# Kernel tuning notes

Hardware: AMD Instinct MI355X
Metric: run time of the kernel (lower is better)

## Reference

```python
import jax, jax.numpy as jnp
import numpy as np
import math

D_MODEL = 1024
NUM_HEADS = 16
D_FF = 4096
EPS = 1e-5
BATCH = 2
SEQ = 2048


def _trunc_normal(key, shape, std):
    # truncated normal on [-3std, 3std], matching nn.init.trunc_normal_
    return std * jax.random.truncated_normal(key, -3.0, 3.0, shape, dtype=jnp.float32)


def setup_inputs() -> dict:
    key = jax.random.key(0)
    ks = jax.random.split(key, 8)
    x = jax.random.normal(ks[0], (BATCH, SEQ, D_MODEL), dtype=jnp.float32)
    std_dd = math.sqrt(2.0 / (D_MODEL + D_MODEL))
    std_up = math.sqrt(2.0 / (D_MODEL + D_FF))
    # Linear stores W as [out_features, in_features]; forward does x @ W.T
    W_q = _trunc_normal(ks[1], (D_MODEL, D_MODEL), std_dd)
    W_k = _trunc_normal(ks[2], (D_MODEL, D_MODEL), std_dd)
    W_v = _trunc_normal(ks[3], (D_MODEL, D_MODEL), std_dd)
    W_o = _trunc_normal(ks[4], (D_MODEL, D_MODEL), std_dd)
    W1 = _trunc_normal(ks[5], (D_FF, D_MODEL), std_up)
    W2 = _trunc_normal(ks[6], (D_MODEL, D_FF), std_up)
    ln1_w = jnp.ones((D_MODEL,), jnp.float32)
    ln1_b = jnp.zeros((D_MODEL,), jnp.float32)
    ln2_w = jnp.ones((D_MODEL,), jnp.float32)
    ln2_b = jnp.zeros((D_MODEL,), jnp.float32)
    return {"x": x, "W_q": W_q, "W_k": W_k, "W_v": W_v, "W_o": W_o,
            "W1": W1, "W2": W2,
            "ln1_w": ln1_w, "ln1_b": ln1_b, "ln2_w": ln2_w, "ln2_b": ln2_b}


def _layernorm(x, w, b):
    xf = x.astype(jnp.float32)
    mean = xf.mean(axis=-1, keepdims=True)
    var = jnp.mean((xf - mean) ** 2, axis=-1, keepdims=True)
    xn = (xf - mean) / jnp.sqrt(var + EPS)
    return (xn * w.astype(jnp.float32) + b.astype(jnp.float32)).astype(x.dtype)


def _attention(x, W_q, W_k, W_v, W_o):
    B, S, D = x.shape
    H, dk = NUM_HEADS, D // NUM_HEADS
    Q = (x @ W_q.T).reshape(B, S, H, dk).transpose(0, 2, 1, 3)  # [B,H,S,dk]
    K = (x @ W_k.T).reshape(B, S, H, dk).transpose(0, 2, 1, 3)
    V = (x @ W_v.T).reshape(B, S, H, dk).transpose(0, 2, 1, 3)
    scores = jnp.einsum('bhqd,bhkd->bhqk', Q, K) / math.sqrt(dk)
    causal = jnp.tril(jnp.ones((S, S), dtype=bool))
    scores = jnp.where(causal, scores, -jnp.inf)
    attn = jax.nn.softmax(scores, axis=-1)
    out = jnp.einsum('bhqk,bhkd->bhqd', attn, V)  # [B,H,S,dk]
    out = out.transpose(0, 2, 1, 3).reshape(B, S, D)
    return out @ W_o.T


def _ffn(x, W1, W2):
    h = x @ W1.T
    h = h * (h > 0)  # ReLU
    return h @ W2.T


def reference(x, W_q, W_k, W_v, W_o, W1, W2, ln1_w, ln1_b, ln2_w, ln2_b):
    x = x + _attention(_layernorm(x, ln1_w, ln1_b), W_q, W_k, W_v, W_o)
    x = x + _ffn(_layernorm(x, ln2_w, ln2_b), W1, W2)
    return x
```

## Files before the change

kernel.cpp:

```cpp
#include <hip/hip_runtime.h>
#include <stdint.h>

typedef unsigned short u16;
typedef unsigned int u32;
typedef __bf16 bf16x8 __attribute__((ext_vector_type(8)));
typedef float f32x4 __attribute__((ext_vector_type(4)));
typedef unsigned short u16x8 __attribute__((ext_vector_type(8)));
typedef unsigned short u16x4 __attribute__((ext_vector_type(4)));
typedef u16x8 u16x8_a __attribute__((may_alias));
typedef u16x4 u16x4_a __attribute__((may_alias));

#define DEV static __device__ __forceinline__

DEV u16 f2bf(float f) {
  unsigned u = __builtin_bit_cast(unsigned, f);
  u += 0x7fffu + ((u >> 16) & 1u);
  return (u16)(u >> 16);
}
DEV bf16x8 ld8(const u16* p) {
  u16x8 v = *(const u16x8_a*)p;
  return __builtin_bit_cast(bf16x8, v);
}
DEV f32x4 vmax4(f32x4 a, f32x4 b) {
  f32x4 r;
  r[0] = fmaxf(a[0], b[0]); r[1] = fmaxf(a[1], b[1]);
  r[2] = fmaxf(a[2], b[2]); r[3] = fmaxf(a[3], b[3]);
  return r;
}
DEV void swz_block(int& bx, int& by) {
  const int gx = gridDim.x;
  const int nwg = gx * gridDim.y;
  int lin = by * gx + bx;
  const int q = nwg >> 3, r = nwg & 7, x = lin & 7, p = lin >> 3;
  lin = (x < r ? x * (q + 1) : r * (q + 1) + (x - r) * q) + p;
  bx = lin % gx; by = lin / gx;
}

#define GL_LDS16(gp, lp)                                                        \
  __builtin_amdgcn_global_load_lds(                                             \
      (const __attribute__((address_space(1))) void*)(gp),                      \
      (__attribute__((address_space(3))) void*)(lp), 16, 0, 0)

#define VMW4 asm volatile("s_waitcnt vmcnt(4)" ::: "memory")
#define VMW2 asm volatile("s_waitcnt vmcnt(2)" ::: "memory")
#define VMW0 asm volatile("s_waitcnt vmcnt(0)" ::: "memory")
#define BAR  __builtin_amdgcn_s_barrier()

struct Cvt6 {
  const float* s[6];
  u16* d[6];
  int n4[6];
};
__global__ __launch_bounds__(256) void cvt6_k(Cvt6 c) {
  const int yi = blockIdx.y;
  const int i = blockIdx.x * 256 + threadIdx.x;
  if (i < c.n4[yi]) {
    float4 v = ((const float4*)c.s[yi])[i];
    u16x4 o;
    o[0] = f2bf(v.x); o[1] = f2bf(v.y); o[2] = f2bf(v.z); o[3] = f2bf(v.w);
    *(u16x4_a*)(c.d[yi] + (size_t)i * 4) = o;
  }
}

__global__ __launch_bounds__(256) void ln_k(const float* __restrict__ x,
                                            const float* __restrict__ w,
                                            const float* __restrict__ b,
                                            u16* __restrict__ o) {
  const int row = blockIdx.x, t = threadIdx.x;
  const float4 v = ((const float4*)(x + (size_t)row * 1024))[t];
  float s = v.x + v.y + v.z + v.w;
  float q = v.x * v.x + v.y * v.y + v.z * v.z + v.w * v.w;
#pragma unroll
  for (int m = 1; m < 64; m <<= 1) { s += __shfl_xor(s, m); q += __shfl_xor(q, m); }
  __shared__ float ss[4], qq[4];
  if ((t & 63) == 0) { ss[t >> 6] = s; qq[t >> 6] = q; }
  __syncthreads();
  s = ss[0] + ss[1] + ss[2] + ss[3];
  q = qq[0] + qq[1] + qq[2] + qq[3];
  const float mean = s * (1.f / 1024.f);
  const float var = q * (1.f / 1024.f) - mean * mean;
  const float rstd = rsqrtf(var + 1e-5f);
  const float4 wv = ((const float4*)w)[t];
  const float4 bv = ((const float4*)b)[t];
  u16x4 ov;
  ov[0] = f2bf((v.x - mean) * rstd * wv.x + bv.x);
  ov[1] = f2bf((v.y - mean) * rstd * wv.y + bv.y);
  ov[2] = f2bf((v.z - mean) * rstd * wv.z + bv.z);
  ov[3] = f2bf((v.w - mean) * rstd * wv.w + bv.w);
  *(u16x4_a*)(o + (size_t)row * 1024 + t * 4) = ov;
}

__global__ __launch_bounds__(256) void vtr_k(const u16* __restrict__ qkvV,
                                             u16* __restrict__ vt) {
  __shared__ u16 T[64][65];
  const int st = blockIdx.x, bh = blockIdx.y;
  const int b = bh >> 4, h = bh & 15;
  const int t = threadIdx.x;
  const u16* src = qkvV + ((size_t)(b * 2048 + st * 64)) * 3072 + h * 64;
  const int r = t >> 2, c0 = (t & 3) * 16;
  u16x8 a0 = *(const u16x8_a*)(src + (size_t)r * 3072 + c0);
  u16x8 a1 = *(const u16x8_a*)(src + (size_t)r * 3072 + c0 + 8);
#pragma unroll
  for (int e = 0; e < 8; ++e) { T[r][c0 + e] = a0[e]; T[r][c0 + 8 + e] = a1[e]; }
  __syncthreads();
  const int d = t >> 2, s0 = (t & 3) * 16;
  u16x8 o0, o1;
#pragma unroll
  for (int e = 0; e < 8; ++e) { o0[e] = T[s0 + e][d]; o1[e] = T[s0 + 8 + e][d]; }
  u16* dst = vt + ((size_t)bh * 64 + d) * 2048 + (size_t)st * 64 + s0;
  *(u16x8_a*)dst = o0;
  *(u16x8_a*)(dst + 8) = o1;
}

DEV void stage_op(const u16* __restrict__ G, int K, int kk, u16* lds, int set,
                  int isB, int w, int l) {
#pragma unroll
  for (int i = 0; i < 2; ++i) {
    const int c = i * 8 + w;
    int rb;
    if (!isB) { const int lr = c * 8; rb = (lr < 64 ? lr : lr + 64) + set * 64; }
    else      { rb = (c >> 2) * 64 + set * 32 + (c & 3) * 8; }
    const int row = rb + (l >> 3);
    const int c8 = (l & 7) ^ (row & 7);
    GL_LDS16(G + (size_t)row * K + kk + c8 * 8, lds + rb * 64);
  }
}
DEV void rdA(const u16* as, int wr, int mh, int l15, int l4, bf16x8 af[4][2]) {
#pragma unroll
  for (int f = 0; f < 4; ++f) {
    const int row = wr * 128 + mh * 64 + f * 16 + l15;
#pragma unroll
    for (int ks = 0; ks < 2; ++ks) {
      const int c8 = (ks * 4 + l4) ^ (row & 7);
      af[f][ks] = ld8(as + row * 64 + c8 * 8);
    }
  }
}
DEV void rdB(const u16* bs, int wc, int nh, int l15, int l4, bf16x8 bf_[2][2]) {
#pragma unroll
  for (int g = 0; g < 2; ++g) {
    const int row = wc * 64 + nh * 32 + g * 16 + l15;
#pragma unroll
    for (int ks = 0; ks < 2; ++ks) {
      const int c8 = (ks * 4 + l4) ^ (row & 7);
      bf_[g][ks] = ld8(bs + row * 64 + c8 * 8);
    }
  }
}

#define MFMA16(mh, nh)                                                          \
  __builtin_amdgcn_s_setprio(1);                                                \
  _Pragma("unroll")                                                             \
  for (int f = 0; f < 4; ++f) {                                                 \
    _Pragma("unroll")                                                           \
    for (int g = 0; g < 2; ++g) {                                               \
      f32x4& a_ = acc[(mh) * 4 + f][(nh) * 2 + g];                              \
      a_ = __builtin_amdgcn_mfma_f32_16x16x32_bf16(af[f][0], bfr[g][0], a_, 0, 0, 0); \
      a_ = __builtin_amdgcn_mfma_f32_16x16x32_bf16(af[f][1], bfr[g][1], a_, 0, 0, 0); \
    }                                                                           \
  }                                                                             \
  __builtin_amdgcn_s_setprio(0);

template <int EPI>
__global__ __launch_bounds__(512, 2) void gemm8(const u16* __restrict__ A,
                                                const u16* __restrict__ Bw,
                                                u16* __restrict__ Cp,
                                                int M, int N, int K, int qcols) {
  __shared__ __align__(16) u16 As[2][256 * 64];
  __shared__ __align__(16) u16 Bs[2][256 * 64];
  const int t = threadIdx.x, w = t >> 6, l = t & 63;
  const int l15 = l & 15, l4 = l >> 4;
  const int wr = w >> 2, wc = w & 3;
  int bx = blockIdx.x, by = blockIdx.y;
  swz_block(bx, by);
  const int bm0 = by * 256, bn0 = bx * 256;
  const u16* Ab = A + (size_t)bm0 * K;
  const u16* Bb = Bw + (size_t)bn0 * K;

  f32x4 acc[8][4] = {};
  stage_op(Ab, K, 0, As[0], 0, 0, w, l);
  stage_op(Bb, K, 0, Bs[0], 0, 1, w, l);
  stage_op(Bb, K, 0, Bs[0], 1, 1, w, l);
  stage_op(Ab, K, 0, As[0], 1, 0, w, l);
  VMW4;
  BAR;

  const int nk = K >> 6;
  int cur = 0;
  bf16x8 af[4][2], bfr[2][2];
  for (int kt = 0; kt < nk; ++kt) {
    const int kn = (kt + 1) << 6;
    const bool more = (kt + 1 < nk);
    u16* An = As[cur ^ 1];
    u16* Bn = Bs[cur ^ 1];
    rdA(As[cur], wr, 0, l15, l4, af);
    rdB(Bs[cur], wc, 0, l15, l4, bfr);
    if (more) stage_op(Ab, K, kn, An, 0, 0, w, l);
    BAR;
    MFMA16(0, 0)
    if (more) { VMW4; } else { VMW2; }
    BAR;
    rdB(Bs[cur], wc, 1, l15, l4, bfr);
    if (more) stage_op(Bb, K, kn, Bn, 0, 1, w, l);
    BAR;
    MFMA16(0, 1)
    if (more) { VMW4; } else { VMW0; }
    BAR;
    rdA(As[cur], wr, 1, l15, l4, af);
    if (more) stage_op(Bb, K, kn, Bn, 1, 1, w, l);
    BAR;
    MFMA16(1, 1)
    BAR;
    rdB(Bs[cur], wc, 0, l15, l4, bfr);
    if (more) stage_op(Ab, K, kn, An, 1, 0, w, l);
    BAR;
    MFMA16(1, 0)
    if (more) { VMW4; }
    BAR;
    cur ^= 1;
  }

#pragma unroll
  for (int m = 0; m < 8; ++m) {
    const int row0 = bm0 + wr * 128 + m * 16 + l4 * 4;
#pragma unroll
    for (int n = 0; n < 4; ++n) {
      const int col = bn0 + wc * 64 + n * 16 + l15;
      const float qs = (col < qcols) ? 0.18033688f : 1.f;
#pragma unroll
      for (int r = 0; r < 4; ++r) {
        float v = acc[m][n][r] * qs;
        if constexpr (EPI == 1) v = v > 0.f ? v : 0.f;
        Cp[(size_t)(row0 + r) * N + col] = f2bf(v);
      }
    }
  }
}

__global__ __launch_bounds__(256, 2) void gemm64(const u16* __restrict__ A,
                                                 const u16* __restrict__ Bw,
                                                 float* __restrict__ C,
                                                 const float* __restrict__ res,
                                                 int M, int N, int K) {
  __shared__ __align__(16) u16 As[2][64 * 64];
  __shared__ __align__(16) u16 Bs[2][128 * 64];
  const int t = threadIdx.x, w = t >> 6, l = t & 63;
  const int l15 = l & 15, l4 = l >> 4;
  const int wr = w >> 1, wc = w & 1;
  int bx = blockIdx.x, by = blockIdx.y;
  swz_block(bx, by);
  const int bm0 = by * 64, bn0 = bx * 128;
  const u16* Ab = A + (size_t)bm0 * K;
  const u16* Bb = Bw + (size_t)bn0 * K;

  auto stgA = [&](int buf, int kk) {
#pragma unroll
    for (int i = 0; i < 2; ++i) {
      const int s = t + i * 256;
      const int row = s >> 3;
      const int c8 = (l & 7) ^ (row & 7);
      GL_LDS16(Ab + (size_t)row * K + kk + c8 * 8, &As[buf][(s >> 6) * 512]);
    }
  };
  auto stgB = [&](int buf, int kk) {
#pragma unroll
    for (int i = 0; i < 4; ++i) {
      const int s = t + i * 256;
      const int row = s >> 3;
      const int c8 = (l & 7) ^ (row & 7);
      GL_LDS16(Bb + (size_t)row * K + kk + c8 * 8, &Bs[buf][(s >> 6) * 512]);
    }
  };

  f32x4 acc[2][4] = {};
  stgA(0, 0); stgB(0, 0);
  const int nk = K >> 6;
  int cur = 0;
  for (int kt = 0; kt < nk; ++kt) {
    __syncthreads();
    if (kt + 1 < nk) { stgA(cur ^ 1, (kt + 1) << 6); stgB(cur ^ 1, (kt + 1) << 6); }
    bf16x8 af[2][2], bfr[4][2];
#pragma unroll
    for (int f = 0; f < 2; ++f) {
      const int row = wr * 32 + f * 16 + l15;
#pragma unroll
      for (int ks = 0; ks < 2; ++ks)
        af[f][ks] = ld8(&As[cur][row * 64 + (((ks * 4 + l4) ^ (row & 7)) * 8)]);
    }
#pragma unroll
    for (int n = 0; n < 4; ++n) {
      const int row = wc * 64 + n * 16 + l15;
#pragma unroll
      for (int ks = 0; ks < 2; ++ks)
        bfr[n][ks] = ld8(&Bs[cur][row * 64 + (((ks * 4 + l4) ^ (row & 7)) * 8)]);
    }
    __builtin_amdgcn_s_setprio(1);
#pragma unroll
    for (int f = 0; f < 2; ++f)
#pragma unroll
      for (int n = 0; n < 4; ++n) {
        acc[f][n] = __builtin_amdgcn_mfma_f32_16x16x32_bf16(af[f][0], bfr[n][0], acc[f][n], 0, 0, 0);
        acc[f][n] = __builtin_amdgcn_mfma_f32_16x16x32_bf16(af[f][1], bfr[n][1], acc[f][n], 0, 0, 0);
      }
    __builtin_amdgcn_s_setprio(0);
    __syncthreads();
    cur ^= 1;
  }

#pragma unroll
  for (int f = 0; f < 2; ++f) {
    const int row0 = bm0 + wr * 32 + f * 16 + l4 * 4;
#pragma unroll
    for (int n = 0; n < 4; ++n) {
      const int col = bn0 + wc * 64 + n * 16 + l15;
#pragma unroll
      for (int r = 0; r < 4; ++r) {
        const size_t idx = (size_t)(row0 + r) * N + col;
        C[idx] = res[idx] + acc[f][n][r];
      }
    }
  }
}

__global__ __launch_bounds__(256) void attn_k(const u16* __restrict__ Qm,
                                              const u16* __restrict__ Km,
                                              const u16* __restrict__ vt,
                                              u16* __restrict__ Om) {
  const int S = 2048, D = 1024, ldq = 3072;
  int p = blockIdx.x, bh = blockIdx.y;
  swz_block(p, bh);
  const int bb = bh >> 4, h = bh & 15;
  const int t = threadIdx.x, w = t >> 6, l = t & 63, l15 = l & 15, l4 = l >> 4;
  const float NEGINF = -__builtin_inff();

  __shared__ __align__(16) u16 Ksm[2][64 * 64];
  __shared__ __align__(16) u16 Vsm[2][64 * 64];
  __shared__ __align__(16) u32 Psm[4][16 * 32];

  const u16* Qb = Qm + (size_t)bb * S * ldq + h * 64;
  const u16* Kb = Km + (size_t)bb * S * ldq + h * 64;
  const u16* Vtb = vt + (size_t)bh * 64 * 2048;

  auto stageKV = [&](int j, int buf) {
    const int k0 = j * 64;
#pragma unroll
    for (int i = 0; i < 2; ++i) {
      const int s = t + i * 256;
      const int row = s >> 3;
      const int colE = ((s & 7) ^ (row & 7)) * 8;
      GL_LDS16(Kb + (size_t)(k0 + row) * ldq + colE, &Ksm[buf][(s >> 6) * 512]);
      GL_LDS16(Vtb + (size_t)row * 2048 + k0 + colE, &Vsm[buf][(s >> 6) * 512]);
    }
  };

  u32* Pw = &Psm[w][0];
  const u16* Pu = (const u16*)Pw;
  const int h7 = l15 & 7;

  for (int half = 0; half < 2; ++half) {
    const int bx = half ? (31 - p) : p;
    const int q0 = bx * 64;
    __syncthreads();
    stageKV(0, 0);

    bf16x8 qf[2];
    const int qq = q0 + w * 16 + l15;
#pragma unroll
    for (int c = 0; c < 2; ++c) qf[c] = ld8(Qb + (size_t)qq * ldq + c * 32 + l4 * 8);

    f32x4 accT[4] = {};
    float mrow = NEGINF, lrow = 0.f;
    int cur = 0;

    for (int j = 0; j <= bx; ++j) {
      __syncthreads();
      if (j < bx) stageKV(j + 1, cur ^ 1);

      f32x4 sv[4] = {};
      __builtin_amdgcn_s_setprio(1);
#pragma unroll
      for (int c = 0; c < 2; ++c) {
#pragma unroll
        for (int nf = 0; nf < 4; ++nf) {
          const int row = nf * 16 + l15;
          bf16x8 kf = ld8(&Ksm[cur][row * 64 + ((c * 32 + l4 * 8) ^ ((row & 7) * 8))]);
          sv[nf] = __builtin_amdgcn_mfma_f32_16x16x32_bf16(kf, qf[c], sv[nf], 0, 0, 0);
        }
      }
      __builtin_amdgcn_s_setprio(0);

      if (j == bx) {
        const int k0 = j * 64;
#pragma unroll
        for (int nf = 0; nf < 4; ++nf) {
          const int kb = k0 + nf * 16 + l4 * 4;
#pragma unroll
          for (int r = 0; r < 4; ++r)
            if (kb + r > qq) sv[nf][r] = NEGINF;
        }
      }

      f32x4 m4 = vmax4(vmax4(sv[0], sv[1]), vmax4(sv[2], sv[3]));
      float mt = fmaxf(fmaxf(m4[0], m4[1]), fmaxf(m4[2], m4[3]));
      mt = fmaxf(mt, __shfl_xor(mt, 16));
      mt = fmaxf(mt, __shfl_xor(mt, 32));
      const bool skip = __all(mt - mrow <= 11.54f);
      const float mnew = skip ? mrow : fmaxf(mrow, mt);
      if (!skip) {
        const float sf = __builtin_amdgcn_exp2f(mrow - mnew);
        lrow *= sf;
#pragma unroll
        for (int nf = 0; nf < 4; ++nf) accT[nf] *= sf;
        mrow = mnew;
      }
#pragma unroll
      for (int nf = 0; nf < 4; ++nf)
#pragma unroll
        for (int r = 0; r < 4; ++r)
          sv[nf][r] = __builtin_amdgcn_exp2f(sv[nf][r] - mnew);
      f32x4 s4 = (sv[0] + sv[1]) + (sv[2] + sv[3]);
      float ps = (s4[0] + s4[1]) + (s4[2] + s4[3]);
      ps += __shfl_xor(ps, 16);
      ps += __shfl_xor(ps, 32);
      lrow += ps;

#pragma unroll
      for (int nf = 0; nf < 4; ++nf) {
        u32 lo, hi;
        asm("v_cvt_pk_bf16_f32 %0, %1, %2" : "=v"(lo) : "v"(sv[nf][0]), "v"(sv[nf][1]));
        asm("v_cvt_pk_bf16_f32 %0, %1, %2" : "=v"(hi) : "v"(sv[nf][2]), "v"(sv[nf][3]));
        const int kw4 = (nf * 2 + (l4 >> 1)) ^ h7;
        const int base = l15 * 32 + kw4 * 4 + (l4 & 1) * 2;
        Pw[base] = lo;
        Pw[base + 1] = hi;
      }

      __builtin_amdgcn_s_setprio(1);
#pragma unroll
      for (int c = 0; c < 2; ++c) {
        bf16x8 pf = ld8(Pu + l15 * 64 + ((c * 4 + l4) ^ h7) * 8);
#pragma unroll
        for (int nf = 0; nf < 4; ++nf) {
          const int row = nf * 16 + l15;
          bf16x8 vf = ld8(&Vsm[cur][row * 64 + ((c * 32 + l4 * 8) ^ ((row & 7) * 8))]);
          accT[nf] = __builtin_amdgcn_mfma_f32_16x16x32_bf16(vf, pf, accT[nf], 0, 0, 0);
        }
      }
      __builtin_amdgcn_s_setprio(0);
      cur ^= 1;
    }

    const float inv = 1.f / lrow;
    u16* orow = Om + ((size_t)bb * S + qq) * D + h * 64;
#pragma unroll
    for (int nf = 0; nf < 4; ++nf) {
      u16x4 ov;
#pragma unroll
      for (int r = 0; r < 4; ++r) ov[r] = f2bf(accT[nf][r] * inv);
      *(u16x4_a*)(orow + nf * 16 + l4 * 4) = ov;
    }
  }
}

extern "C" void kernel_launch(void* const* d_in, const int* in_sizes, int n_in,
                              void* d_out, int out_size, void* d_ws, size_t ws_size,
                              hipStream_t stream) {
  (void)in_sizes; (void)n_in; (void)out_size; (void)ws_size;
  const float* x    = (const float*)d_in[0];
  const float* W_q  = (const float*)d_in[1];
  const float* W_k  = (const float*)d_in[2];
  const float* W_v  = (const float*)d_in[3];
  const float* W_o  = (const float*)d_in[4];
  const float* W1   = (const float*)d_in[5];
  const float* W2   = (const float*)d_in[6];
  const float* ln1w = (const float*)d_in[7];
  const float* ln1b = (const float*)d_in[8];
  const float* ln2w = (const float*)d_in[9];
  const float* ln2b = (const float*)d_in[10];

  const size_t MB = 1ull << 20;
  char* W = (char*)d_ws;
  u16* wqkv  = (u16*)(W + 0);
  u16* wo    = (u16*)(W + 6 * MB);
  u16* w1b   = (u16*)(W + 8 * MB);
  u16* w2b   = (u16*)(W + 16 * MB);
  u16* xn1   = (u16*)(W + 24 * MB);
  u16* qkv   = (u16*)(W + 32 * MB);
  u16* attnb = (u16*)(W + 56 * MB);
  u16* vt    = (u16*)(W + 64 * MB);
  u16* xn2   = (u16*)(W + 64 * MB);
  u16* hbuf  = (u16*)(W + 24 * MB);
  float* x2  = (float*)d_out;

  Cvt6 c;
  c.s[0] = W_q; c.d[0] = wqkv;              c.n4[0] = 1 << 18;
  c.s[1] = W_k; c.d[1] = wqkv + (1 << 20);  c.n4[1] = 1 << 18;
  c.s[2] = W_v; c.d[2] = wqkv + (2 << 20);  c.n4[2] = 1 << 18;
  c.s[3] = W_o; c.d[3] = wo;                c.n4[3] = 1 << 18;
  c.s[4] = W1;  c.d[4] = w1b;               c.n4[4] = 1 << 20;
  c.s[5] = W2;  c.d[5] = w2b;               c.n4[5] = 1 << 20;
  cvt6_k<<<dim3(4096, 6), dim3(256), 0, stream>>>(c);

  ln_k<<<dim3(4096), dim3(256), 0, stream>>>(x, ln1w, ln1b, xn1);
  gemm8<0><<<dim3(12, 16), dim3(512), 0, stream>>>(xn1, wqkv, qkv, 4096, 3072, 1024, 1024);
  vtr_k<<<dim3(32, 32), dim3(256), 0, stream>>>(qkv + 2048, vt);
  attn_k<<<dim3(16, 32), dim3(256), 0, stream>>>(qkv, qkv + 1024, vt, attnb);
  gemm64<<<dim3(8, 64), dim3(256), 0, stream>>>(attnb, wo, x2, x, 4096, 1024, 1024);
  ln_k<<<dim3(4096), dim3(256), 0, stream>>>(x2, ln2w, ln2b, xn2);
  gemm8<1><<<dim3(16, 16), dim3(512), 0, stream>>>(xn2, w1b, hbuf, 4096, 4096, 1024, 0);
  gemm64<<<dim3(8, 64), dim3(256), 0, stream>>>(hbuf, w2b, x2, x2, 4096, 1024, 4096);
}
```

Measured before the change: 224.7 us.

## Use 128x128 split-K GEMM with separate reduction for FFN down projection

Replaces the 64-tile GEMM for the FFN down projection with a 128x128-tile kernel that splits K into two halves across blockIdx.z. The first K-half writes the residual-added result, the second writes a float partial buffer, and a new elementwise kernel adds the partial into the output. This aims to raise data reuse per tile while keeping enough blocks to fill the GPU. It costs an extra 16MB partial write, a reduction pass and one extra launch.

New measurement: 228.7 us. Within noise of the previous version (+1.8%).

```diff
diff --git a/kernel.cpp b/kernel.cpp
--- a/kernel.cpp
+++ b/kernel.cpp
@@ -59,6 +59,17 @@
     u16x4 o;
     o[0] = f2bf(v.x); o[1] = f2bf(v.y); o[2] = f2bf(v.z); o[3] = f2bf(v.w);
     *(u16x4_a*)(c.d[yi] + (size_t)i * 4) = o;
+  }
+}
+
+__global__ __launch_bounds__(256) void red_k(const float* __restrict__ p,
+                                             float* __restrict__ d, int n4) {
+  int i = blockIdx.x * 256 + threadIdx.x;
+  if (i < n4) {
+    float4 a = ((const float4*)d)[i];
+    float4 b = ((const float4*)p)[i];
+    a.x += b.x; a.y += b.y; a.z += b.z; a.w += b.w;
+    ((float4*)d)[i] = a;
   }
 }
 
@@ -322,6 +333,88 @@
   }
 }
 
+__global__ __launch_bounds__(256, 2) void gemm128s(const u16* __restrict__ A,
+                                                   const u16* __restrict__ Bw,
+                                                   float* __restrict__ C,
+                                                   float* __restrict__ P,
+                                                   const float* __restrict__ res,
+                                                   int M, int N, int K, int Kc) {
+  __shared__ __align__(16) u16 As[2][128 * 64];
+  __shared__ __align__(16) u16 Bs[2][128 * 64];
+  const int t = threadIdx.x, w = t >> 6, l = t & 63;
+  const int l15 = l & 15, l4 = l >> 4;
+  const int wr = w >> 1, wc = w & 1;
+  int bx = blockIdx.x, by = blockIdx.y;
+  swz_block(bx, by);
+  const int kz = blockIdx.z;
+  const int bm0 = by * 128, bn0 = bx * 128;
+  const u16* Ab = A + (size_t)bm0 * K + (size_t)kz * Kc;
+  const u16* Bb = Bw + (size_t)bn0 * K + (size_t)kz * Kc;
+
+  auto stg = [&](const u16* __restrict__ G, u16* lds, int kk) {
+#pragma unroll
+    for (int i = 0; i < 4; ++i) {
+      const int s = t + i * 256;
+      const int row = s >> 3;
+      const int c8 = (l & 7) ^ (row & 7);
+      GL_LDS16(G + (size_t)row * K + kk + c8 * 8, lds + (s >> 6) * 512);
+    }
+  };
+
+  f32x4 acc[4][4] = {};
+  stg(Ab, As[0], 0); stg(Bb, Bs[0], 0);
+  const int nk = Kc >> 6;
+  int cur = 0;
+  for (int kt = 0; kt < nk; ++kt) {
+    __syncthreads();
+    if (kt + 1 < nk) {
+      stg(Ab, As[cur ^ 1], (kt + 1) << 6);
+      stg(Bb, Bs[cur ^ 1], (kt + 1) << 6);
+    }
+    bf16x8 af[4][2], bfr[4][2];
+#pragma unroll
+    for (int f = 0; f < 4; ++f) {
+      const int row = wr * 64 + f * 16 + l15;
+#pragma unroll
+      for (int ks = 0; ks < 2; ++ks)
+        af[f][ks] = ld8(&As[cur][row * 64 + (((ks * 4 + l4) ^ (row & 7)) * 8)]);
+    }
+#pragma unroll
+    for (int n = 0; n < 4; ++n) {
+      const int row = wc * 64 + n * 16 + l15;
+#pragma unroll
+      for (int ks = 0; ks < 2; ++ks)
+        bfr[n][ks] = ld8(&Bs[cur][row * 64 + (((ks * 4 + l4) ^ (row & 7)) * 8)]);
+    }
+    __builtin_amdgcn_s_setprio(1);
+#pragma unroll
+    for (int f = 0; f < 4; ++f)
+#pragma unroll
+      for (int n = 0; n < 4; ++n) {
+        acc[f][n] = __builtin_amdgcn_mfma_f32_16x16x32_bf16(af[f][0], bfr[n][0], acc[f][n], 0, 0, 0);
+        acc[f][n] = __builtin_amdgcn_mfma_f32_16x16x32_bf16(af[f][1], bfr[n][1], acc[f][n], 0, 0, 0);
+      }
+    __builtin_amdgcn_s_setprio(0);
+    __syncthreads();
+    cur ^= 1;
+  }
+
+#pragma unroll
+  for (int f = 0; f < 4; ++f) {
+    const int row0 = bm0 + wr * 64 + f * 16 + l4 * 4;
+#pragma unroll
+    for (int n = 0; n < 4; ++n) {
+      const int col = bn0 + wc * 64 + n * 16 + l15;
+#pragma unroll
+      for (int r = 0; r < 4; ++r) {
+        const size_t idx = (size_t)(row0 + r) * N + col;
+        if (kz == 0) C[idx] = res[idx] + acc[f][n][r];
+        else         P[idx] = acc[f][n][r];
+      }
+    }
+  }
+}
+
 __global__ __launch_bounds__(256) void attn_k(const u16* __restrict__ Qm,
                                               const u16* __restrict__ Km,
                                               const u16* __restrict__ vt,
@@ -490,6 +583,7 @@
   u16* vt    = (u16*)(W + 64 * MB);
   u16* xn2   = (u16*)(W + 64 * MB);
   u16* hbuf  = (u16*)(W + 24 * MB);
+  float* fpart = (float*)(W + 56 * MB);
   float* x2  = (float*)d_out;
 
   Cvt6 c;
@@ -508,5 +602,7 @@
   gemm64<<<dim3(8, 64), dim3(256), 0, stream>>>(attnb, wo, x2, x, 4096, 1024, 1024);
   ln_k<<<dim3(4096), dim3(256), 0, stream>>>(x2, ln2w, ln2b, xn2);
   gemm8<1><<<dim3(16, 16), dim3(512), 0, stream>>>(xn2, w1b, hbuf, 4096, 4096, 1024, 0);
-  gemm64<<<dim3(8, 64), dim3(256), 0, stream>>>(hbuf, w2b, x2, x2, 4096, 1024, 4096);
-}
+  gemm128s<<<dim3(8, 32, 2), dim3(256), 0, stream>>>(hbuf, w2b, x2, fpart, x2,
+                                                     4096, 1024, 4096, 2048);
+  red_k<<<dim3(4096), dim3(256), 0, stream>>>(fpart, x2, 1 << 20);
+}
```
